# Kernel tuning notes

Hardware: AMD Instinct MI355X
Metric: run time of the kernel (lower is better)

## Reference

```python
import jax, jax.numpy as jnp
import numpy as np

DIL = 2  # dilation of the 3x3 neighborhood (hardcoded in the torch module)
# 8 non-center neighbor offsets of a dilated 3x3 kernel
_OFFSETS = [(-DIL, -DIL), (-DIL, 0), (-DIL, DIL),
            (0, -DIL),              (0, DIL),
            (DIL, -DIL), (DIL, 0),  (DIL, DIL)]


def setup_inputs() -> dict:
    key = jax.random.key(0)
    k1, k2 = jax.random.split(key)
    shape = (16, 1, 1024, 1024)
    y_true = jax.random.uniform(k1, shape, dtype=jnp.float32)
    y_pred = jax.random.uniform(k2, shape, dtype=jnp.float32)
    return {"y_true": y_true, "y_pred": y_pred}


def reference(y_true, y_pred):
    # --- BCE with torch's log clamp at -100 (reduction='none') ---
    log_p  = jnp.maximum(jnp.log(y_pred),   -100.0)
    log_1p = jnp.maximum(jnp.log1p(-y_pred), -100.0)
    a = -(y_true * log_p + (1.0 - y_true) * log_1p)

    # --- detached copy (y_pred.clone().detach()) ---
    sloss = jax.lax.stop_gradient(y_pred)

    # --- max |center - neighbor| over 8 dilated neighbors, zero-padded borders ---
    H, W = sloss.shape[2], sloss.shape[3]
    padded = jnp.pad(sloss, ((0, 0), (0, 0), (DIL, DIL), (DIL, DIL)))
    unfolded_weights = jnp.zeros_like(sloss)
    for dy, dx in _OFFSETS:
        nb = padded[:, :, DIL + dy:DIL + dy + H, DIL + dx:DIL + dx + W]
        unfolded_weights = jnp.maximum(unfolded_weights, jnp.abs(sloss - nb))

    # thred[thred < 0.5] = 0; loss1 uses thred BEFORE the >=0.5 -> 1 assignment
    thred = jnp.where(sloss >= 0.5, sloss, 0.0)
    loss = unfolded_weights * thred + a
    return loss.mean()
```

## Files before the change

kernel.cpp:

```cpp
#include <hip/hip_runtime.h>

#define HH 1024
#define WW 1024
#define NB 16
#define TR 8
#define SR (TR + 4)
#define NBLK (NB * (HH / TR))
#define NELEM ((long long)NB * HH * WW)

__device__ __forceinline__ void lds_win(const float* __restrict__ S, int row,
                                        int c0, bool ledge, bool redge, float w[8]) {
    const float* p = S + row * WW;
    float2 L = *(const float2*)(p + (ledge ? c0 : c0 - 2));
    float4 M = *(const float4*)(p + c0);
    float2 R = *(const float2*)(p + (redge ? c0 : c0 + 4));
    if (ledge) { L.x = 0.f; L.y = 0.f; }
    if (redge) { R.x = 0.f; R.y = 0.f; }
    w[0]=L.x; w[1]=L.y; w[2]=M.x; w[3]=M.y; w[4]=M.z; w[5]=M.w; w[6]=R.x; w[7]=R.y;
}

__global__ __launch_bounds__(256) void closs_main(const float* __restrict__ yt,
                                                  const float* __restrict__ yp,
                                                  float* __restrict__ partial) {
    __shared__ float S[SR * WW];

    const int bid  = blockIdx.x;
    const int img  = bid >> 7;
    const int tile = bid & 127;
    const int y0   = tile * TR;
    const int tid  = threadIdx.x;
    const int c0   = tid << 2;

    const float* __restrict__ ybase = yp + (long long)img * (HH * WW);
    const float* __restrict__ tbase = yt + ((long long)img * HH + y0) * WW;

#pragma unroll
    for (int i = 0; i < SR; ++i) {
        const int gy = y0 - 2 + i;
        float4 v = make_float4(0.f, 0.f, 0.f, 0.f);
        if (gy >= 0 && gy < HH)
            v = *(const float4*)(ybase + gy * WW + c0);
        *(float4*)&S[i * WW + c0] = v;
    }
    __syncthreads();

    const bool ledge = (tid == 0);
    const bool redge = (tid == 255);

    float sum = 0.f;
#pragma unroll
    for (int k = 0; k < TR; ++k) {
        float A[8], B[8], C[8];
        lds_win(S, k,     c0, ledge, redge, A);
        lds_win(S, k + 2, c0, ledge, redge, B);
        lds_win(S, k + 4, c0, ledge, redge, C);

        const float4 t4 = *(const float4*)(tbase + k * WW + c0);
        const float tt[4] = {t4.x, t4.y, t4.z, t4.w};

#pragma unroll
        for (int j = 0; j < 4; ++j) {
            const float c = B[j + 2];
            const float mxA = fmaxf(fmaxf(A[j], A[j + 2]), A[j + 4]);
            const float mxB = fmaxf(B[j], B[j + 4]);
            const float mxC = fmaxf(fmaxf(C[j], C[j + 2]), C[j + 4]);
            const float mx  = fmaxf(fmaxf(mxA, mxB), mxC);
            const float mnA = fminf(fminf(A[j], A[j + 2]), A[j + 4]);
            const float mnB = fminf(B[j], B[j + 4]);
            const float mnC = fminf(fminf(C[j], C[j + 2]), C[j + 4]);
            const float mn  = fminf(fminf(mnA, mnB), mnC);
            const float w   = fmaxf(mx - c, c - mn);

            const float lp  = fmaxf(__logf(c), -100.f);
            const float l1p = fmaxf(__logf(1.f - c), -100.f);
            const float th  = (c >= 0.5f) ? c : 0.f;
            sum += w * th - l1p - tt[j] * (lp - l1p);
        }
    }

    for (int o = 32; o > 0; o >>= 1) sum += __shfl_down(sum, o);
    __shared__ float wsum[4];
    if ((tid & 63) == 0) wsum[tid >> 6] = sum;
    __syncthreads();
    if (tid == 0) partial[bid] = wsum[0] + wsum[1] + wsum[2] + wsum[3];
}

__global__ __launch_bounds__(1024) void closs_reduce(const float* __restrict__ partial,
                                                     float* __restrict__ out) {
    const float2* p2 = (const float2*)partial;
    float2 v = p2[threadIdx.x];
    float s = v.x + v.y;
    for (int o = 32; o > 0; o >>= 1) s += __shfl_down(s, o);
    __shared__ float wsum[16];
    if ((threadIdx.x & 63) == 0) wsum[threadIdx.x >> 6] = s;
    __syncthreads();
    if (threadIdx.x == 0) {
        float t = 0.f;
#pragma unroll
        for (int i = 0; i < 16; ++i) t += wsum[i];
        out[0] = t * (1.0f / (float)NELEM);
    }
}

extern "C" void kernel_launch(void* const* d_in, const int* in_sizes, int n_in,
                              void* d_out, int out_size, void* d_ws, size_t ws_size,
                              hipStream_t stream) {
    const float* y_true = (const float*)d_in[0];
    const float* y_pred = (const float*)d_in[1];
    float* out = (float*)d_out;
    float* partial = (float*)d_ws;

    closs_main<<<NBLK, 256, 0, stream>>>(y_true, y_pred, partial);
    closs_reduce<<<1, 1024, 0, stream>>>(partial, out);
}
```

Before: 146.2 us.

## Replace LDS row staging with register-rotated global row windows

Removes the 48KB shared-memory tile and its block-wide sync. Each thread now loads its 8-wide row windows straight from global memory and keeps two interleaved rolling register sets (even and odd rows) for the dilation-2 stencil. It also adds a 4-blocks-per-CU occupancy hint. The trade-off is that the overlapping halo reads now go through L1/L2 instead of being served from LDS, which may raise cache traffic and register pressure.

```diff
diff --git a/kernel.cpp b/kernel.cpp
--- a/kernel.cpp
+++ b/kernel.cpp
@@ -4,26 +4,52 @@
 #define WW 1024
 #define NB 16
 #define TR 8
-#define SR (TR + 4)
 #define NBLK (NB * (HH / TR))
 #define NELEM ((long long)NB * HH * WW)
 
-__device__ __forceinline__ void lds_win(const float* __restrict__ S, int row,
-                                        int c0, bool ledge, bool redge, float w[8]) {
-    const float* p = S + row * WW;
-    float2 L = *(const float2*)(p + (ledge ? c0 : c0 - 2));
-    float4 M = *(const float4*)(p + c0);
-    float2 R = *(const float2*)(p + (redge ? c0 : c0 + 4));
-    if (ledge) { L.x = 0.f; L.y = 0.f; }
-    if (redge) { R.x = 0.f; R.y = 0.f; }
-    w[0]=L.x; w[1]=L.y; w[2]=M.x; w[3]=M.y; w[4]=M.z; w[5]=M.w; w[6]=R.x; w[7]=R.y;
+__device__ __forceinline__ void gwin(const float* __restrict__ ybase, int gy,
+                                     int c0, bool ledge, bool redge, float w[8]) {
+    if (gy >= 0 && gy < HH) {
+        const float* r = ybase + gy * WW;
+        float2 L = *(const float2*)(r + (ledge ? c0 : c0 - 2));
+        float4 M = *(const float4*)(r + c0);
+        float2 R = *(const float2*)(r + (redge ? c0 : c0 + 4));
+        if (ledge) { L.x = 0.f; L.y = 0.f; }
+        if (redge) { R.x = 0.f; R.y = 0.f; }
+        w[0]=L.x; w[1]=L.y; w[2]=M.x; w[3]=M.y; w[4]=M.z; w[5]=M.w; w[6]=R.x; w[7]=R.y;
+    } else {
+#pragma unroll
+        for (int i = 0; i < 8; ++i) w[i] = 0.f;
+    }
 }
 
-__global__ __launch_bounds__(256) void closs_main(const float* __restrict__ yt,
-                                                  const float* __restrict__ yp,
-                                                  float* __restrict__ partial) {
-    __shared__ float S[SR * WW];
+__device__ __forceinline__ void row4(const float A[8], const float B[8],
+                                     const float C[8], const float4 t4,
+                                     float& sum) {
+    const float tt[4] = {t4.x, t4.y, t4.z, t4.w};
+#pragma unroll
+    for (int j = 0; j < 4; ++j) {
+        const float c = B[j + 2];
+        const float mxA = fmaxf(fmaxf(A[j], A[j + 2]), A[j + 4]);
+        const float mxB = fmaxf(B[j], B[j + 4]);
+        const float mxC = fmaxf(fmaxf(C[j], C[j + 2]), C[j + 4]);
+        const float mx  = fmaxf(fmaxf(mxA, mxB), mxC);
+        const float mnA = fminf(fminf(A[j], A[j + 2]), A[j + 4]);
+        const float mnB = fminf(B[j], B[j + 4]);
+        const float mnC = fminf(fminf(C[j], C[j + 2]), C[j + 4]);
+        const float mn  = fminf(fminf(mnA, mnB), mnC);
+        const float w   = fmaxf(mx - c, c - mn);
 
+        const float lp  = fmaxf(__logf(c), -100.f);
+        const float l1p = fmaxf(__logf(1.f - c), -100.f);
+        const float th  = (c >= 0.5f) ? c : 0.f;
+        sum += w * th - l1p - tt[j] * (lp - l1p);
+    }
+}
+
+__global__ __launch_bounds__(256, 4) void closs_main(const float* __restrict__ yt,
+                                                     const float* __restrict__ yp,
+                                                     float* __restrict__ partial) {
     const int bid  = blockIdx.x;
     const int img  = bid >> 7;
     const int tile = bid & 127;
@@ -31,50 +57,32 @@
     const int tid  = threadIdx.x;
     const int c0   = tid << 2;
 
+    const bool ledge = (tid == 0);
+    const bool redge = (tid == 255);
+
     const float* __restrict__ ybase = yp + (long long)img * (HH * WW);
     const float* __restrict__ tbase = yt + ((long long)img * HH + y0) * WW;
 
-#pragma unroll
-    for (int i = 0; i < SR; ++i) {
-        const int gy = y0 - 2 + i;
-        float4 v = make_float4(0.f, 0.f, 0.f, 0.f);
-        if (gy >= 0 && gy < HH)
-            v = *(const float4*)(ybase + gy * WW + c0);
-        *(float4*)&S[i * WW + c0] = v;
-    }
-    __syncthreads();
-
-    const bool ledge = (tid == 0);
-    const bool redge = (tid == 255);
+    float Ae[8], Be[8], Ce[8], Ao[8], Bo[8], Co[8];
+    gwin(ybase, y0 - 2, c0, ledge, redge, Ae);
+    gwin(ybase, y0,     c0, ledge, redge, Be);
+    gwin(ybase, y0 - 1, c0, ledge, redge, Ao);
+    gwin(ybase, y0 + 1, c0, ledge, redge, Bo);
 
     float sum = 0.f;
 #pragma unroll
     for (int k = 0; k < TR; ++k) {
-        float A[8], B[8], C[8];
-        lds_win(S, k,     c0, ledge, redge, A);
-        lds_win(S, k + 2, c0, ledge, redge, B);
-        lds_win(S, k + 4, c0, ledge, redge, C);
-
         const float4 t4 = *(const float4*)(tbase + k * WW + c0);
-        const float tt[4] = {t4.x, t4.y, t4.z, t4.w};
-
+        if ((k & 1) == 0) {
+            gwin(ybase, y0 + k + 2, c0, ledge, redge, Ce);
+            row4(Ae, Be, Ce, t4, sum);
 #pragma unroll
-        for (int j = 0; j < 4; ++j) {
-            const float c = B[j + 2];
-            const float mxA = fmaxf(fmaxf(A[j], A[j + 2]), A[j + 4]);
-            const float mxB = fmaxf(B[j], B[j + 4]);
-            const float mxC = fmaxf(fmaxf(C[j], C[j + 2]), C[j + 4]);
-            const float mx  = fmaxf(fmaxf(mxA, mxB), mxC);
-            const float mnA = fminf(fminf(A[j], A[j + 2]), A[j + 4]);
-            const float mnB = fminf(B[j], B[j + 4]);
-            const float mnC = fminf(fminf(C[j], C[j + 2]), C[j + 4]);
-            const float mn  = fminf(fminf(mnA, mnB), mnC);
-            const float w   = fmaxf(mx - c, c - mn);
-
-            const float lp  = fmaxf(__logf(c), -100.f);
-            const float l1p = fmaxf(__logf(1.f - c), -100.f);
-            const float th  = (c >= 0.5f) ? c : 0.f;
-            sum += w * th - l1p - tt[j] * (lp - l1p);
+            for (int i = 0; i < 8; ++i) { Ae[i] = Be[i]; Be[i] = Ce[i]; }
+        } else {
+            gwin(ybase, y0 + k + 2, c0, ledge, redge, Co);
+            row4(Ao, Bo, Co, t4, sum);
+#pragma unroll
+            for (int i = 0; i < 8; ++i) { Ao[i] = Bo[i]; Bo[i] = Co[i]; }
         }
     }
 
```

After: 157.4 us. +7.6%, slower.

## Replace LDS staging with direct global-memory sliding row windows in registers

Applied to the files above, without the earlier changes.

Removes the 48KB shared-memory tile and its barrier. Each thread now loads its 8-wide row window straight from global memory, using float2/float4 loads that include the dilated halo, and keeps a sliding set of rows in registers so each row is loaded once. It also sets a launch-bounds occupancy hint of 4 blocks per CU. The aim is to drop the LDS capacity limit on occupancy and the LDS round trip. The cost is redundant global and L2 traffic for the overlapping halo loads, plus higher register pressure.

```diff
diff --git a/kernel.cpp b/kernel.cpp
--- a/kernel.cpp
+++ b/kernel.cpp
@@ -4,26 +4,51 @@
 #define WW 1024
 #define NB 16
 #define TR 8
-#define SR (TR + 4)
 #define NBLK (NB * (HH / TR))
 #define NELEM ((long long)NB * HH * WW)
 
-__device__ __forceinline__ void lds_win(const float* __restrict__ S, int row,
-                                        int c0, bool ledge, bool redge, float w[8]) {
-    const float* p = S + row * WW;
-    float2 L = *(const float2*)(p + (ledge ? c0 : c0 - 2));
-    float4 M = *(const float4*)(p + c0);
-    float2 R = *(const float2*)(p + (redge ? c0 : c0 + 4));
-    if (ledge) { L.x = 0.f; L.y = 0.f; }
-    if (redge) { R.x = 0.f; R.y = 0.f; }
-    w[0]=L.x; w[1]=L.y; w[2]=M.x; w[3]=M.y; w[4]=M.z; w[5]=M.w; w[6]=R.x; w[7]=R.y;
-}
+#define GWIN(gy, p) \
+    float p##0, p##1, p##2, p##3, p##4, p##5, p##6, p##7; \
+    { const int _gy = (gy); \
+      if (_gy >= 0 && _gy < HH) { \
+        const float* _r = ybase + _gy * WW; \
+        float2 _L = *(const float2*)(_r + (ledge ? c0 : c0 - 2)); \
+        float4 _M = *(const float4*)(_r + c0); \
+        float2 _R = *(const float2*)(_r + (redge ? c0 : c0 + 4)); \
+        if (ledge) { _L.x = 0.f; _L.y = 0.f; } \
+        if (redge) { _R.x = 0.f; _R.y = 0.f; } \
+        p##0 = _L.x; p##1 = _L.y; p##2 = _M.x; p##3 = _M.y; \
+        p##4 = _M.z; p##5 = _M.w; p##6 = _R.x; p##7 = _R.y; \
+      } else { \
+        p##0 = 0.f; p##1 = 0.f; p##2 = 0.f; p##3 = 0.f; \
+        p##4 = 0.f; p##5 = 0.f; p##6 = 0.f; p##7 = 0.f; } }
 
-__global__ __launch_bounds__(256) void closs_main(const float* __restrict__ yt,
-                                                  const float* __restrict__ yp,
-                                                  float* __restrict__ partial) {
-    __shared__ float S[SR * WW];
+#define COL(al, am, ar, bl, bm, br, cl, cm, cr, tt) { \
+    const float c   = bm; \
+    const float mxA = fmaxf(fmaxf(al, am), ar); \
+    const float mxB = fmaxf(bl, br); \
+    const float mxC = fmaxf(fmaxf(cl, cm), cr); \
+    const float mx  = fmaxf(fmaxf(mxA, mxB), mxC); \
+    const float mnA = fminf(fminf(al, am), ar); \
+    const float mnB = fminf(bl, br); \
+    const float mnC = fminf(fminf(cl, cm), cr); \
+    const float mn  = fminf(fminf(mnA, mnB), mnC); \
+    const float w   = fmaxf(mx - c, c - mn); \
+    const float lp  = fmaxf(__logf(c), -100.f); \
+    const float l1p = fmaxf(__logf(1.f - c), -100.f); \
+    const float th  = (c >= 0.5f) ? c : 0.f; \
+    sum += w * th - l1p - (tt) * (lp - l1p); }
 
+#define ROW4(A, B, C, k) { \
+    const float4 _t = *(const float4*)(tbase + (k) * WW + c0); \
+    COL(A##0, A##2, A##4, B##0, B##2, B##4, C##0, C##2, C##4, _t.x); \
+    COL(A##1, A##3, A##5, B##1, B##3, B##5, C##1, C##3, C##5, _t.y); \
+    COL(A##2, A##4, A##6, B##2, B##4, B##6, C##2, C##4, C##6, _t.z); \
+    COL(A##3, A##5, A##7, B##3, B##5, B##7, C##3, C##5, C##7, _t.w); }
+
+__global__ __launch_bounds__(256, 4) void closs_main(const float* __restrict__ yt,
+                                                     const float* __restrict__ yp,
+                                                     float* __restrict__ partial) {
     const int bid  = blockIdx.x;
     const int img  = bid >> 7;
     const int tile = bid & 127;
@@ -31,52 +56,34 @@
     const int tid  = threadIdx.x;
     const int c0   = tid << 2;
 
+    const bool ledge = (tid == 0);
+    const bool redge = (tid == 255);
+
     const float* __restrict__ ybase = yp + (long long)img * (HH * WW);
     const float* __restrict__ tbase = yt + ((long long)img * HH + y0) * WW;
 
-#pragma unroll
-    for (int i = 0; i < SR; ++i) {
-        const int gy = y0 - 2 + i;
-        float4 v = make_float4(0.f, 0.f, 0.f, 0.f);
-        if (gy >= 0 && gy < HH)
-            v = *(const float4*)(ybase + gy * WW + c0);
-        *(float4*)&S[i * WW + c0] = v;
-    }
-    __syncthreads();
+    float sum = 0.f;
 
-    const bool ledge = (tid == 0);
-    const bool redge = (tid == 255);
-
-    float sum = 0.f;
-#pragma unroll
-    for (int k = 0; k < TR; ++k) {
-        float A[8], B[8], C[8];
-        lds_win(S, k,     c0, ledge, redge, A);
-        lds_win(S, k + 2, c0, ledge, redge, B);
-        lds_win(S, k + 4, c0, ledge, redge, C);
-
-        const float4 t4 = *(const float4*)(tbase + k * WW + c0);
-        const float tt[4] = {t4.x, t4.y, t4.z, t4.w};
-
-#pragma unroll
-        for (int j = 0; j < 4; ++j) {
-            const float c = B[j + 2];
-            const float mxA = fmaxf(fmaxf(A[j], A[j + 2]), A[j + 4]);
-            const float mxB = fmaxf(B[j], B[j + 4]);
-            const float mxC = fmaxf(fmaxf(C[j], C[j + 2]), C[j + 4]);
-            const float mx  = fmaxf(fmaxf(mxA, mxB), mxC);
-            const float mnA = fminf(fminf(A[j], A[j + 2]), A[j + 4]);
-            const float mnB = fminf(B[j], B[j + 4]);
-            const float mnC = fminf(fminf(C[j], C[j + 2]), C[j + 4]);
-            const float mn  = fminf(fminf(mnA, mnB), mnC);
-            const float w   = fmaxf(mx - c, c - mn);
-
-            const float lp  = fmaxf(__logf(c), -100.f);
-            const float l1p = fmaxf(__logf(1.f - c), -100.f);
-            const float th  = (c >= 0.5f) ? c : 0.f;
-            sum += w * th - l1p - tt[j] * (lp - l1p);
-        }
-    }
+    GWIN(y0 - 2, ra)
+    GWIN(y0 - 1, rb)
+    GWIN(y0 + 0, rc)
+    GWIN(y0 + 1, rd)
+    GWIN(y0 + 2, re)
+    ROW4(ra, rc, re, 0)
+    GWIN(y0 + 3, rf)
+    ROW4(rb, rd, rf, 1)
+    GWIN(y0 + 4, rg)
+    ROW4(rc, re, rg, 2)
+    GWIN(y0 + 5, rh)
+    ROW4(rd, rf, rh, 3)
+    GWIN(y0 + 6, ri)
+    ROW4(re, rg, ri, 4)
+    GWIN(y0 + 7, rj)
+    ROW4(rf, rh, rj, 5)
+    GWIN(y0 + 8, rk)
+    ROW4(rg, ri, rk, 6)
+    GWIN(y0 + 9, rl)
+    ROW4(rh, rj, rl, 7)
 
     for (int o = 32; o > 0; o >>= 1) sum += __shfl_down(sum, o);
     __shared__ float wsum[4];
```

Result: slower. 155.1 us (+6.0%).
